# Optimization experiments

Hardware: AMD Instinct MI355X
Metric: run time of the kernel (lower is better)

Reference implementation:

```python
import jax, jax.numpy as jnp
import numpy as np

B, N, HID, NSEG = 16, 2048, 32, 3


def _cdist(p):
    # p: [..., N, 3] -> pairwise L2 distances [..., N, N] (matmul expansion)
    sq = jnp.sum(p * p, axis=-1)
    d2 = sq[..., :, None] + sq[..., None, :] - 2.0 * jnp.einsum('...nd,...md->...nm', p, p)
    d2 = jnp.maximum(d2, 0.0)
    return jnp.where(d2 > 0, jnp.sqrt(jnp.maximum(d2, 1e-12)), 0.0)


def _rigid_t(alpha, trans, center, sz):
    # alpha, trans: [B, NSEG, 3]
    c, s = jnp.cos(alpha), jnp.sin(alpha)
    b, t, _ = trans.shape
    z = jnp.zeros((b, t), alpha.dtype)
    o = jnp.ones((b, t), alpha.dtype)
    X = jnp.stack([c[..., 0], -s[..., 0], z, s[..., 0], c[..., 0], z, z, z, o], 2).reshape(b, t, 3, 3)
    Y = jnp.stack([c[..., 1], z, s[..., 1], z, o, z, -s[..., 1], z, c[..., 1]], 2).reshape(b, t, 3, 3)
    Z = jnp.stack([o, z, z, z, c[..., 2], -s[..., 2], z, s[..., 2], c[..., 2]], 2).reshape(b, t, 3, 3)
    XYZ = jnp.einsum('btmn,btnk,btks->btms', X, Y, Z)
    eye = jnp.eye(3, dtype=alpha.dtype)
    T = trans * sz[None, None, :] + jnp.einsum('m,btms->bts', center, eye[None, None] - XYZ)
    return XYZ, T


def _forward(x, W1, b1, W2, b2, A, center, sz):
    Bc, _, Nc = x.shape
    pos = x[:, :3, :]                                   # [B, 3, N]
    h = jax.nn.relu(pos.reshape(Bc, 3 * Nc) @ W1.T + b1)
    z_l = jnp.tanh(h @ W2.T + b2).reshape(Bc, NSEG, 6)
    # Faithful to source: both angles and translation use z_l[:, :, 3:]
    alpha = jnp.pi * z_l[:, :, 3:]
    trans = z_l[:, :, 3:]
    R, T = _rigid_t(alpha, trans, center, sz)           # [B,NSEG,3,3], [B,NSEG,3]
    # per-point segment id (contiguous tessellation), static numpy
    seg = np.concatenate([np.zeros(20, np.int32), np.ones(20, np.int32), np.full(Nc - 40, 2, np.int32)])
    Rp = R[:, seg]                                      # [B, N, 3, 3]
    Tp = T[:, seg]                                      # [B, N, 3]
    # einsum('bkt,bkn->btn', R, x) applied per point (= R^T x + T)
    pos_t = jnp.einsum('bnkt,bkn->btn', Rp, pos) + Tp.transpose(0, 2, 1)
    colors = jax.nn.softmax(x[:, 3:6, :], axis=1)
    X_t = jnp.concatenate([pos_t, colors], axis=1)      # [B, 6, N]
    # regularizer: Frobenius norm of atlas-vs-transformed-input distance mismatch
    dA = _cdist(A[:3, :].T)                             # [N, N]
    dx = _cdist(pos.transpose(0, 2, 1))                 # [B, N, N]
    diff = dA[None] - dx
    reg = jnp.sqrt(jnp.sum(diff * diff, axis=(1, 2)))   # [B]
    return X_t, reg


def setup_inputs() -> dict:
    key = jax.random.key(0)
    ks = jax.random.split(key, 6)
    x = jax.random.normal(ks[0], (B, 6, N), jnp.float32)
    W1 = jax.random.normal(ks[1], (HID, 3 * N), jnp.float32) * 0.02
    b1 = jax.random.normal(ks[2], (HID,), jnp.float32) * 0.02
    W2 = jax.random.normal(ks[3], (6 * NSEG, HID), jnp.float32) * 0.02
    b2 = jax.random.normal(ks[4], (6 * NSEG,), jnp.float32) * 0.02
    A = jax.random.normal(ks[5], (6, N), jnp.float32)
    sz = jnp.array([256.0, 256.0, 64.0], jnp.float32)
    center = sz / 2.0
    return {"x": x, "W1": W1, "b1": b1, "W2": W2, "b2": b2, "A": A,
            "center": center, "sz": sz, "times": 1}


def reference(x, W1, b1, W2, b2, A, center, sz, times):
    # `times` is accepted but unused, as in the original forward
    return _forward(x, W1, b1, W2, b2, A, center, sz)
```

## Files before the change

### kernel.cpp

```cpp
#include <hip/hip_runtime.h>
#include <hip/hip_bf16.h>

#define NPTS 2048
#define BATCH 16
#define REG_BASE 196608

#define H_OFF     0
#define MOM_OFF   512
#define CROSS_OFF 580
#define CNT_OFF   596
#define POSW_OFF  640
#define AW_OFF    (POSW_OFF + 16*2048*4)
#define WS_FLOATS (AW_OFF + 2048*4)
#define WS_BYTES  ((size_t)WS_FLOATS * 4)

#define CBLKS 576

__device__ __forceinline__ float rl(float v, int k) {
    return __int_as_float(__builtin_amdgcn_readlane(__float_as_int(v), k));
}


__global__ __launch_bounds__(256) void k_h(
    const float* __restrict__ x, const float* __restrict__ W1,
    const float* __restrict__ b1, float* __restrict__ ws)
{
    const int jg = blockIdx.x, b = blockIdx.y;
    const int t = threadIdx.x;
    const int j = jg * 8 + (t >> 5);
    const int l = t & 31;

    if (jg == 0 && b == 0 && t < 85)
        ws[MOM_OFF + t] = 0.f;

    const float4* xb4 = reinterpret_cast<const float4*>(x + (size_t)b * 12288);
    const float4* wj4 = reinterpret_cast<const float4*>(W1 + (size_t)j * 6144);
    float dot = 0.f;
    #pragma unroll 4
    for (int k = l; k < 1536; k += 32) {
        float4 a = xb4[k];
        float4 w = wj4[k];
        dot += a.x * w.x + a.y * w.y + a.z * w.z + a.w * w.w;
    }
    dot += __shfl_xor(dot, 1, 32);
    dot += __shfl_xor(dot, 2, 32);
    dot += __shfl_xor(dot, 4, 32);
    dot += __shfl_xor(dot, 8, 32);
    dot += __shfl_xor(dot, 16, 32);
    if (l == 0) ws[H_OFF + b * 32 + j] = fmaxf(dot + b1[j], 0.f);
}

__global__ __launch_bounds__(256) void k_transform(
    const float* __restrict__ x, const float* __restrict__ A,
    const float* __restrict__ W2, const float* __restrict__ b2,
    const float* __restrict__ center, const float* __restrict__ sz,
    float* __restrict__ out, float* __restrict__ ws)
{
    const int c = blockIdx.x, b = blockIdx.y;
    const int t = threadIdx.x;
    const int n = c * 256 + t;
    float4* posw = reinterpret_cast<float4*>(ws + POSW_OFF);
    float4* aw   = reinterpret_cast<float4*>(ws + AW_OFF);

    __shared__ float zs[3][3];
    __shared__ float Rl[3][9];
    __shared__ float Tl[3][3];

    float px, py, pz;
    if (b < BATCH) {
        if (t < 9) {
            const int s = t / 3, d = t % 3;
            const float* hb = ws + H_OFF + b * 32;
            const int row = s * 6 + 3 + d;
            float acc = b2[row];
            #pragma unroll
            for (int jj = 0; jj < 32; ++jj) acc += hb[jj] * W2[row * 32 + jj];
            zs[s][d] = tanhf(acc);
        }
        __syncthreads();
        if (t < 3) {
            const int s = t;
            const float PI = 3.14159265358979323846f;
            float c0 = cosf(PI * zs[s][0]), s0 = sinf(PI * zs[s][0]);
            float c1 = cosf(PI * zs[s][1]), s1 = sinf(PI * zs[s][1]);
            float c2 = cosf(PI * zs[s][2]), s2 = sinf(PI * zs[s][2]);
            float X[3][3] = {{c0, -s0, 0.f}, {s0, c0, 0.f}, {0.f, 0.f, 1.f}};
            float Y[3][3] = {{c1, 0.f, s1}, {0.f, 1.f, 0.f}, {-s1, 0.f, c1}};
            float Z[3][3] = {{1.f, 0.f, 0.f}, {0.f, c2, -s2}, {0.f, s2, c2}};
            float YZ[3][3], M[3][3];
            for (int m = 0; m < 3; ++m)
                for (int nn = 0; nn < 3; ++nn) {
                    float v = 0.f;
                    for (int k = 0; k < 3; ++k) v += Y[m][k] * Z[k][nn];
                    YZ[m][nn] = v;
                }
            for (int m = 0; m < 3; ++m)
                for (int nn = 0; nn < 3; ++nn) {
                    float v = 0.f;
                    for (int k = 0; k < 3; ++k) v += X[m][k] * YZ[k][nn];
                    M[m][nn] = v;
                    Rl[s][m * 3 + nn] = v;
                }
            for (int d = 0; d < 3; ++d)
                Tl[s][d] = zs[s][d] * sz[d] + center[d]
                         - (center[0] * M[0][d] + center[1] * M[1][d] + center[2] * M[2][d]);
        }
        __syncthreads();

        const float* xb = x + (size_t)b * 12288;
        px = xb[n]; py = xb[2048 + n]; pz = xb[4096 + n];
        posw[b * 2048 + n] = make_float4(px, py, pz, 0.f);

        const int s = (n < 20) ? 0 : (n < 40) ? 1 : 2;
        float* ob = out + (size_t)b * 12288;
        #pragma unroll
        for (int d = 0; d < 3; ++d)
            ob[d * 2048 + n] = Rl[s][0 * 3 + d] * px + Rl[s][1 * 3 + d] * py
                             + Rl[s][2 * 3 + d] * pz + Tl[s][d];

        float c3 = xb[6144 + n], c4 = xb[8192 + n], c5 = xb[10240 + n];
        float mx = fmaxf(c3, fmaxf(c4, c5));
        float e3 = __expf(c3 - mx), e4 = __expf(c4 - mx), e5 = __expf(c5 - mx);
        float inv = 1.f / (e3 + e4 + e5);
        ob[6144 + n] = e3 * inv;
        ob[8192 + n] = e4 * inv;
        ob[10240 + n] = e5 * inv;
    } else {
        px = A[n]; py = A[2048 + n]; pz = A[4096 + n];
        aw[n] = make_float4(px, py, pz, 0.f);
    }

    float v0 = px, v1 = py, v2 = pz, v3 = px * px + py * py + pz * pz;
    #pragma unroll
    for (int m = 1; m < 64; m <<= 1) {
        v0 += __shfl_xor(v0, m);
        v1 += __shfl_xor(v1, m);
        v2 += __shfl_xor(v2, m);
        v3 += __shfl_xor(v3, m);
    }
    __shared__ float wpart[4][4];
    const int w = t >> 6;
    if ((t & 63) == 0) {
        wpart[w][0] = v0; wpart[w][1] = v1; wpart[w][2] = v2; wpart[w][3] = v3;
    }
    __syncthreads();
    if (t < 4) {
        float s4 = wpart[0][t] + wpart[1][t] + wpart[2][t] + wpart[3][t];
        atomicAdd(&ws[MOM_OFF + b * 4 + t], s4);
    }
}

__global__ __launch_bounds__(256) void k_cross(
    float* __restrict__ ws, float* __restrict__ out)
{
    const int bx = blockIdx.x;
    const int tile = bx % 144;
    const int b0 = (bx / 144) * 4;
    int rem = tile, ci = 0;
    while (rem >= 32 - 4 * ci) { rem -= 32 - 4 * ci; ++ci; }
    const int cj = 4 * ci + rem;
    const int t = threadIdx.x;
    const int ln = t & 63;
    const int i = ci * 256 + t;
    const int jb = cj * 64;

    const float4* posw = reinterpret_cast<const float4*>(ws + POSW_OFF);
    const float4* aw   = reinterpret_cast<const float4*>(ws + AW_OFF);

    const float4 Ai  = aw[i];
    const float4 Aj  = aw[jb + ln];
    const float4 Pi0 = posw[(size_t)(b0 + 0) * 2048 + i];
    const float4 Pi1 = posw[(size_t)(b0 + 1) * 2048 + i];
    const float4 Pi2 = posw[(size_t)(b0 + 2) * 2048 + i];
    const float4 Pi3 = posw[(size_t)(b0 + 3) * 2048 + i];
    const float4 Pj0 = posw[(size_t)(b0 + 0) * 2048 + jb + ln];
    const float4 Pj1 = posw[(size_t)(b0 + 1) * 2048 + jb + ln];
    const float4 Pj2 = posw[(size_t)(b0 + 2) * 2048 + jb + ln];
    const float4 Pj3 = posw[(size_t)(b0 + 3) * 2048 + jb + ln];

    float a0 = 0.f, a1 = 0.f, a2 = 0.f, a3 = 0.f;

#define CROSS_ONE(PI, PJ, ACC)                                              \
    {                                                                       \
        float ux = PI.x - rl(PJ.x, k);                                      \
        float uy = PI.y - rl(PJ.y, k);                                      \
        float uz = PI.z - rl(PJ.z, k);                                      \
        float d2x = ux * ux + uy * uy + uz * uz;                            \
        float s = __builtin_amdgcn_sqrtf(d2x * d2a);                        \
        if (PRED) s = (jb + k > i) ? s : 0.f;                               \
        ACC += s;                                                           \
    }
#define CROSS_STEP                                                          \
    {                                                                       \
        float qx = rl(Aj.x, k), qy = rl(Aj.y, k), qz = rl(Aj.z, k);         \
        float vx = Ai.x - qx, vy = Ai.y - qy, vz = Ai.z - qz;               \
        float d2a = vx * vx + vy * vy + vz * vz;                            \
        CROSS_ONE(Pi0, Pj0, a0)                                             \
        CROSS_ONE(Pi1, Pj1, a1)                                             \
        CROSS_ONE(Pi2, Pj2, a2)                                             \
        CROSS_ONE(Pi3, Pj3, a3)                                             \
    }

    if (rem < 4) {
        #define PRED true
        #pragma unroll 8
        for (int k = 0; k < 64; ++k) CROSS_STEP
        #undef PRED
    } else {
        #define PRED false
        #pragma unroll 8
        for (int k = 0; k < 64; ++k) CROSS_STEP
        #undef PRED
    }
#undef CROSS_STEP
#undef CROSS_ONE

    #pragma unroll
    for (int m = 1; m < 64; m <<= 1) {
        a0 += __shfl_xor(a0, m);
        a1 += __shfl_xor(a1, m);
        a2 += __shfl_xor(a2, m);
        a3 += __shfl_xor(a3, m);
    }
    __shared__ float wsum[4][4];
    if (ln == 0) {
        const int w = t >> 6;
        wsum[w][0] = a0; wsum[w][1] = a1; wsum[w][2] = a2; wsum[w][3] = a3;
    }
    __syncthreads();
    if (t == 0) {
        #pragma unroll
        for (int q = 0; q < 4; ++q) {
            float s = wsum[0][q] + wsum[1][q] + wsum[2][q] + wsum[3][q];
            atomicAdd(&ws[CROSS_OFF + b0 + q], s);
        }
        __threadfence();
        unsigned old = atomicAdd(reinterpret_cast<unsigned*>(&ws[CNT_OFF]), 1u);
        if (old == CBLKS - 1) {
            __threadfence();
            const float* ma = ws + MOM_OFF + 16 * 4;
            float S2a = 2.f * (2048.f * ma[3] - (ma[0]*ma[0] + ma[1]*ma[1] + ma[2]*ma[2]));
            for (int b = 0; b < BATCH; ++b) {
                const float* mb = ws + MOM_OFF + b * 4;
                float S2x = 2.f * (2048.f * mb[3] - (mb[0]*mb[0] + mb[1]*mb[1] + mb[2]*mb[2]));
                float cr = atomicAdd(&ws[CROSS_OFF + b], 0.f);
                out[REG_BASE + b] = sqrtf(fmaxf(S2a + S2x - 4.f * cr, 0.f));
            }
        }
    }
}

__global__ __launch_bounds__(256) void k_mlp_fb(
    const float* __restrict__ x, const float* __restrict__ W1,
    const float* __restrict__ b1, const float* __restrict__ W2,
    const float* __restrict__ b2, const float* __restrict__ center,
    const float* __restrict__ sz, float* __restrict__ out)
{
    const int b = blockIdx.x;
    const int t = threadIdx.x;
    __shared__ float hbuf[32];
    __shared__ float zbuf[18];
    __shared__ float Rl[3][9];
    __shared__ float Tl[3][3];
    {
        const int j = t >> 3;
        const int l = t & 7;
        const float4* xb4 = reinterpret_cast<const float4*>(x + (size_t)b * 12288);
        const float4* wj4 = reinterpret_cast<const float4*>(W1 + (size_t)j * 6144);
        float dot = 0.f;
        #pragma unroll 4
        for (int k = l; k < 1536; k += 8) {
            float4 a = xb4[k];
            float4 w = wj4[k];
            dot += a.x * w.x + a.y * w.y + a.z * w.z + a.w * w.w;
        }
        dot += __shfl_xor(dot, 1);
        dot += __shfl_xor(dot, 2);
        dot += __shfl_xor(dot, 4);
        if (l == 0) hbuf[j] = fmaxf(dot + b1[j], 0.f);
    }
    if (t == 0) out[REG_BASE + b] = 0.f;
    __syncthreads();
    if (t < 18) {
        float s = b2[t];
        #pragma unroll
        for (int j = 0; j < 32; ++j) s += hbuf[j] * W2[t * 32 + j];
        zbuf[t] = tanhf(s);
    }
    __syncthreads();
    if (t < 3) {
        const int s = t;
        const float PI = 3.14159265358979323846f;
        float a0 = PI * zbuf[s * 6 + 3], a1 = PI * zbuf[s * 6 + 4], a2 = PI * zbuf[s * 6 + 5];
        float c0 = cosf(a0), s0 = sinf(a0);
        float c1 = cosf(a1), s1 = sinf(a1);
        float c2 = cosf(a2), s2 = sinf(a2);
        float X[3][3] = {{c0, -s0, 0.f}, {s0, c0, 0.f}, {0.f, 0.f, 1.f}};
        float Y[3][3] = {{c1, 0.f, s1}, {0.f, 1.f, 0.f}, {-s1, 0.f, c1}};
        float Z[3][3] = {{1.f, 0.f, 0.f}, {0.f, c2, -s2}, {0.f, s2, c2}};
        float YZ[3][3], M[3][3];
        for (int m = 0; m < 3; ++m)
            for (int n = 0; n < 3; ++n) {
                float v = 0.f;
                for (int k = 0; k < 3; ++k) v += Y[m][k] * Z[k][n];
                YZ[m][n] = v;
            }
        for (int m = 0; m < 3; ++m)
            for (int n = 0; n < 3; ++n) {
                float v = 0.f;
                for (int k = 0; k < 3; ++k) v += X[m][k] * YZ[k][n];
                M[m][n] = v;
                Rl[s][m * 3 + n] = v;
            }
        for (int sd = 0; sd < 3; ++sd)
            Tl[s][sd] = zbuf[s * 6 + 3 + sd] * sz[sd] + center[sd]
                      - (center[0] * M[0][sd] + center[1] * M[1][sd] + center[2] * M[2][sd]);
    }
    __syncthreads();
    const float* xb = x + (size_t)b * 12288;
    float* ob = out + (size_t)b * 12288;
    for (int n = t; n < 2048; n += 256) {
        float px = xb[n], py = xb[2048 + n], pz = xb[4096 + n];
        int s = (n < 20) ? 0 : (n < 40) ? 1 : 2;
        #pragma unroll
        for (int td = 0; td < 3; ++td)
            ob[td * 2048 + n] = Rl[s][0 * 3 + td] * px + Rl[s][1 * 3 + td] * py
                              + Rl[s][2 * 3 + td] * pz + Tl[s][td];
        float c3 = xb[6144 + n], c4 = xb[8192 + n], c5 = xb[10240 + n];
        float mx = fmaxf(c3, fmaxf(c4, c5));
        float e3 = __expf(c3 - mx), e4 = __expf(c4 - mx), e5 = __expf(c5 - mx);
        float inv = 1.f / (e3 + e4 + e5);
        ob[6144 + n] = e3 * inv;
        ob[8192 + n] = e4 * inv;
        ob[10240 + n] = e5 * inv;
    }
}

__global__ __launch_bounds__(256) void k_reg_fb(
    const float* __restrict__ x, const float* __restrict__ A,
    float* __restrict__ out)
{
    const int p = blockIdx.x;
    const int b = blockIdx.y;
    int ci = 0, rem = p;
    while (rem >= 8 - ci) { rem -= 8 - ci; ++ci; }
    const int cj = ci + rem;
    const int t = threadIdx.x;
    __shared__ float4 pj[256];
    __shared__ float4 aj[256];
    const float* xb = x + (size_t)b * 12288;
    {
        int j = cj * 256 + t;
        pj[t] = make_float4(xb[j], xb[2048 + j], xb[4096 + j], 0.f);
        aj[t] = make_float4(A[j], A[2048 + j], A[4096 + j], 0.f);
    }
    __syncthreads();
    const int i = ci * 256 + t;
    const float pix = xb[i], piy = xb[2048 + i], piz = xb[4096 + i];
    const float aix = A[i], aiy = A[2048 + i], aiz = A[4096 + i];
    const int jbase = cj * 256;
    float acc = 0.f;
    #pragma unroll 4
    for (int jj = 0; jj < 256; ++jj) {
        float4 P = pj[jj];
        float4 Q = aj[jj];
        float dx0 = pix - P.x, dy0 = piy - P.y, dz0 = piz - P.z;
        float dxv = sqrtf(dx0 * dx0 + dy0 * dy0 + dz0 * dz0);
        float da0 = aix - Q.x, da1 = aiy - Q.y, da2 = aiz - Q.z;
        float dav = sqrtf(da0 * da0 + da1 * da1 + da2 * da2);
        float d = dav - dxv;
        float dd = (jbase + jj > i) ? d : 0.f;
        acc = fmaf(dd, dd, acc);
    }
    #pragma unroll
    for (int m = 1; m < 64; m <<= 1) acc += __shfl_xor(acc, m);
    __shared__ float wsum[4];
    if ((t & 63) == 0) wsum[t >> 6] = acc;
    __syncthreads();
    if (t == 0) atomicAdd(&out[REG_BASE + b], wsum[0] + wsum[1] + wsum[2] + wsum[3]);
}

__global__ void k_final_fb(float* __restrict__ out)
{
    int b = threadIdx.x;
    if (b < BATCH) out[REG_BASE + b] = sqrtf(2.f * out[REG_BASE + b]);
}

extern "C" void kernel_launch(void* const* d_in, const int* in_sizes, int n_in,
                              void* d_out, int out_size, void* d_ws, size_t ws_size,
                              hipStream_t stream) {
    (void)in_sizes; (void)n_in; (void)out_size;
    const float* x      = (const float*)d_in[0];
    const float* W1     = (const float*)d_in[1];
    const float* b1     = (const float*)d_in[2];
    const float* W2     = (const float*)d_in[3];
    const float* b2     = (const float*)d_in[4];
    const float* A      = (const float*)d_in[5];
    const float* center = (const float*)d_in[6];
    const float* sz     = (const float*)d_in[7];
    float* out = (float*)d_out;
    float* ws  = (float*)d_ws;

    if (ws_size >= WS_BYTES) {
        k_h<<<dim3(4, 16), 256, 0, stream>>>(x, W1, b1, ws);
        k_transform<<<dim3(8, 17), 256, 0, stream>>>(x, A, W2, b2, center, sz, out, ws);
        k_cross<<<CBLKS, 256, 0, stream>>>(ws, out);
    } else {
        k_mlp_fb<<<BATCH, 256, 0, stream>>>(x, W1, b1, W2, b2, center, sz, out);
        k_reg_fb<<<dim3(36, 16), 256, 0, stream>>>(x, A, out);
        k_final_fb<<<1, 64, 0, stream>>>(out);
    }
}
```

Measured before the change: 122.8 us.

## Interleave atlas and batch positions into 64-byte rows read via uniform scalar loads

k_transform now writes the atlas point and four batches' positions for each point into one interleaved 16-float row per batch group. k_cross then reads the j-side data through a wave-uniform pointer (readfirstlane), so the loads can go through the scalar path instead of v_readlane broadcasts. The tile size drops from 64 to 32 j-columns, so twice as many blocks run (1152). The aim is to remove per-step readlane VALU overhead and raise parallelism. The cost is more workspace traffic from duplicating the atlas four times, and smaller tiles with more atomics per block.

```diff
diff --git a/kernel.cpp b/kernel.cpp
--- a/kernel.cpp
+++ b/kernel.cpp
@@ -5,19 +5,21 @@
 #define BATCH 16
 #define REG_BASE 196608
 
-#define H_OFF     0
-#define MOM_OFF   512
-#define CROSS_OFF 580
-#define CNT_OFF   596
-#define POSW_OFF  640
-#define AW_OFF    (POSW_OFF + 16*2048*4)
-#define WS_FLOATS (AW_OFF + 2048*4)
-#define WS_BYTES  ((size_t)WS_FLOATS * 4)
-
-#define CBLKS 576
-
-__device__ __forceinline__ float rl(float v, int k) {
-    return __int_as_float(__builtin_amdgcn_readlane(__float_as_int(v), k));
+#define H_OFF      0
+#define MOM_OFF    512
+#define CROSS_OFF  580
+#define CNT_OFF    596
+#define STREAM_OFF 640
+#define WS_FLOATS  (STREAM_OFF + 4*2048*16)
+#define WS_BYTES   ((size_t)WS_FLOATS * 4)
+
+#define CBLKS 1152
+
+__device__ __forceinline__ const float* uni(const float* p) {
+    unsigned long long u = (unsigned long long)p;
+    unsigned lo = __builtin_amdgcn_readfirstlane((unsigned)u);
+    unsigned hi = __builtin_amdgcn_readfirstlane((unsigned)(u >> 32));
+    return (const float*)(((unsigned long long)hi << 32) | lo);
 }
 
 
@@ -59,8 +61,6 @@
     const int c = blockIdx.x, b = blockIdx.y;
     const int t = threadIdx.x;
     const int n = c * 256 + t;
-    float4* posw = reinterpret_cast<float4*>(ws + POSW_OFF);
-    float4* aw   = reinterpret_cast<float4*>(ws + AW_OFF);
 
     __shared__ float zs[3][3];
     __shared__ float Rl[3][9];
@@ -109,7 +109,9 @@
 
         const float* xb = x + (size_t)b * 12288;
         px = xb[n]; py = xb[2048 + n]; pz = xb[4096 + n];
-        posw[b * 2048 + n] = make_float4(px, py, pz, 0.f);
+
+        float* srow = ws + STREAM_OFF + ((size_t)((b >> 2) * 2048 + n) * 16) + 4 + 3 * (b & 3);
+        srow[0] = px; srow[1] = py; srow[2] = pz;
 
         const int s = (n < 20) ? 0 : (n < 40) ? 1 : 2;
         float* ob = out + (size_t)b * 12288;
@@ -127,7 +129,11 @@
         ob[10240 + n] = e5 * inv;
     } else {
         px = A[n]; py = A[2048 + n]; pz = A[4096 + n];
-        aw[n] = make_float4(px, py, pz, 0.f);
+        #pragma unroll
+        for (int g = 0; g < 4; ++g) {
+            float* srow = ws + STREAM_OFF + ((size_t)(g * 2048 + n) * 16);
+            srow[0] = px; srow[1] = py; srow[2] = pz;
+        }
     }
 
     float v0 = px, v1 = py, v2 = pz, v3 = px * px + py * py + pz * pz;
@@ -151,69 +157,66 @@
 }
 
 __global__ __launch_bounds__(256) void k_cross(
-    float* __restrict__ ws, float* __restrict__ out)
+    const float* __restrict__ stream, float* __restrict__ ws,
+    float* __restrict__ out)
 {
     const int bx = blockIdx.x;
-    const int tile = bx % 144;
-    const int b0 = (bx / 144) * 4;
-    int rem = tile, ci = 0;
-    while (rem >= 32 - 4 * ci) { rem -= 32 - 4 * ci; ++ci; }
-    const int cj = 4 * ci + rem;
+    const int g = bx / 288;
+    int rem = bx % 288, ci = 0;
+    while (rem >= 64 - 8 * ci) { rem -= 64 - 8 * ci; ++ci; }
+    const int cj = 8 * ci + rem;
+    const bool diag = (rem < 8);
     const int t = threadIdx.x;
-    const int ln = t & 63;
     const int i = ci * 256 + t;
-    const int jb = cj * 64;
-
-    const float4* posw = reinterpret_cast<const float4*>(ws + POSW_OFF);
-    const float4* aw   = reinterpret_cast<const float4*>(ws + AW_OFF);
-
-    const float4 Ai  = aw[i];
-    const float4 Aj  = aw[jb + ln];
-    const float4 Pi0 = posw[(size_t)(b0 + 0) * 2048 + i];
-    const float4 Pi1 = posw[(size_t)(b0 + 1) * 2048 + i];
-    const float4 Pi2 = posw[(size_t)(b0 + 2) * 2048 + i];
-    const float4 Pi3 = posw[(size_t)(b0 + 3) * 2048 + i];
-    const float4 Pj0 = posw[(size_t)(b0 + 0) * 2048 + jb + ln];
-    const float4 Pj1 = posw[(size_t)(b0 + 1) * 2048 + jb + ln];
-    const float4 Pj2 = posw[(size_t)(b0 + 2) * 2048 + jb + ln];
-    const float4 Pj3 = posw[(size_t)(b0 + 3) * 2048 + jb + ln];
+    const int jb = cj * 32;
+    const int b0 = g * 4;
+
+    const float4* si4 = reinterpret_cast<const float4*>(stream + ((size_t)(g * 2048 + i) * 16));
+    float4 r0 = si4[0], r1 = si4[1], r2 = si4[2], r3 = si4[3];
+    const float aix = r0.x, aiy = r0.y, aiz = r0.z;
+    const float p0x = r1.x, p0y = r1.y, p0z = r1.z;
+    const float p1x = r1.w, p1y = r2.x, p1z = r2.y;
+    const float p2x = r2.z, p2y = r2.w, p2z = r3.x;
+    const float p3x = r3.y, p3y = r3.z, p3z = r3.w;
+
+    const float* sj = uni(stream + ((size_t)(g * 2048 + jb) * 16));
 
     float a0 = 0.f, a1 = 0.f, a2 = 0.f, a3 = 0.f;
 
-#define CROSS_ONE(PI, PJ, ACC)                                              \
-    {                                                                       \
-        float ux = PI.x - rl(PJ.x, k);                                      \
-        float uy = PI.y - rl(PJ.y, k);                                      \
-        float uz = PI.z - rl(PJ.z, k);                                      \
-        float d2x = ux * ux + uy * uy + uz * uz;                            \
-        float s = __builtin_amdgcn_sqrtf(d2x * d2a);                        \
-        if (PRED) s = (jb + k > i) ? s : 0.f;                               \
-        ACC += s;                                                           \
-    }
-#define CROSS_STEP                                                          \
-    {                                                                       \
-        float qx = rl(Aj.x, k), qy = rl(Aj.y, k), qz = rl(Aj.z, k);         \
-        float vx = Ai.x - qx, vy = Ai.y - qy, vz = Ai.z - qz;               \
-        float d2a = vx * vx + vy * vy + vz * vz;                            \
-        CROSS_ONE(Pi0, Pj0, a0)                                             \
-        CROSS_ONE(Pi1, Pj1, a1)                                             \
-        CROSS_ONE(Pi2, Pj2, a2)                                             \
-        CROSS_ONE(Pi3, Pj3, a3)                                             \
-    }
-
-    if (rem < 4) {
-        #define PRED true
-        #pragma unroll 8
-        for (int k = 0; k < 64; ++k) CROSS_STEP
-        #undef PRED
+#define CROSS_K(PRED)                                                        \
+    {                                                                        \
+        const float4* q4 = reinterpret_cast<const float4*>(sj + k * 16);     \
+        float4 qa = q4[0], qb = q4[1], qc = q4[2], qd = q4[3];               \
+        float vx = aix - qa.x, vy = aiy - qa.y, vz = aiz - qa.z;             \
+        float d2a = fmaf(vx, vx, fmaf(vy, vy, vz * vz));                     \
+        float u0x = p0x - qb.x, u0y = p0y - qb.y, u0z = p0z - qb.z;          \
+        float d20 = fmaf(u0x, u0x, fmaf(u0y, u0y, u0z * u0z));               \
+        float u1x = p1x - qb.w, u1y = p1y - qc.x, u1z = p1z - qc.y;          \
+        float d21 = fmaf(u1x, u1x, fmaf(u1y, u1y, u1z * u1z));               \
+        float u2x = p2x - qc.z, u2y = p2y - qc.w, u2z = p2z - qd.x;          \
+        float d22 = fmaf(u2x, u2x, fmaf(u2y, u2y, u2z * u2z));               \
+        float u3x = p3x - qd.y, u3y = p3y - qd.z, u3z = p3z - qd.w;          \
+        float d23 = fmaf(u3x, u3x, fmaf(u3y, u3y, u3z * u3z));               \
+        float s0 = __builtin_amdgcn_sqrtf(d20 * d2a);                        \
+        float s1 = __builtin_amdgcn_sqrtf(d21 * d2a);                        \
+        float s2 = __builtin_amdgcn_sqrtf(d22 * d2a);                        \
+        float s3 = __builtin_amdgcn_sqrtf(d23 * d2a);                        \
+        if (PRED) {                                                          \
+            bool ok = (jb + k > i);                                          \
+            s0 = ok ? s0 : 0.f; s1 = ok ? s1 : 0.f;                          \
+            s2 = ok ? s2 : 0.f; s3 = ok ? s3 : 0.f;                          \
+        }                                                                    \
+        a0 += s0; a1 += s1; a2 += s2; a3 += s3;                              \
+    }
+
+    if (diag) {
+        #pragma unroll 4
+        for (int k = 0; k < 32; ++k) CROSS_K(true)
     } else {
-        #define PRED false
-        #pragma unroll 8
-        for (int k = 0; k < 64; ++k) CROSS_STEP
-        #undef PRED
-    }
-#undef CROSS_STEP
-#undef CROSS_ONE
+        #pragma unroll 4
+        for (int k = 0; k < 32; ++k) CROSS_K(false)
+    }
+#undef CROSS_K
 
     #pragma unroll
     for (int m = 1; m < 64; m <<= 1) {
@@ -223,7 +226,7 @@
         a3 += __shfl_xor(a3, m);
     }
     __shared__ float wsum[4][4];
-    if (ln == 0) {
+    if ((t & 63) == 0) {
         const int w = t >> 6;
         wsum[w][0] = a0; wsum[w][1] = a1; wsum[w][2] = a2; wsum[w][3] = a3;
     }
@@ -404,7 +407,7 @@
     if (ws_size >= WS_BYTES) {
         k_h<<<dim3(4, 16), 256, 0, stream>>>(x, W1, b1, ws);
         k_transform<<<dim3(8, 17), 256, 0, stream>>>(x, A, W2, b2, center, sz, out, ws);
-        k_cross<<<CBLKS, 256, 0, stream>>>(ws, out);
+        k_cross<<<CBLKS, 256, 0, stream>>>(ws + STREAM_OFF, ws, out);
     } else {
         k_mlp_fb<<<BATCH, 256, 0, stream>>>(x, W1, b1, W2, b2, center, sz, out);
         k_reg_fb<<<dim3(36, 16), 256, 0, stream>>>(x, A, out);
```

After: 159.5 us. +30.0%, slower.
